# Kernel optimization log

Hardware: AMD Instinct MI355X
Metric: run time of the kernel (lower is better)

Reference implementation:

```python
import jax, jax.numpy as jnp
import numpy as np

N_NODES = 50000
N_GRAPHS = 128


def gcn_conv(x, W, b, src, dst, n_nodes):
    """PyG-style GCNConv: add self-loops, symmetric normalization, linear transform, scatter-add."""
    # linear transform first (PyG applies lin before propagate)
    h = x @ W  # [N, out]
    loop = jnp.arange(n_nodes, dtype=src.dtype)
    src_f = jnp.concatenate([src, loop])  # [E+N]
    dst_f = jnp.concatenate([dst, loop])
    # degree over destination (incl. self-loops), edge weight = 1
    deg = jax.ops.segment_sum(jnp.ones_like(src_f, dtype=h.dtype), dst_f, num_segments=n_nodes)
    dinv = jnp.where(deg > 0, jax.lax.rsqrt(deg), 0.0)
    norm = dinv[src_f] * dinv[dst_f]  # [E+N]
    msg = h[src_f] * norm[:, None]  # gather + scale
    out = jax.ops.segment_sum(msg, dst_f, num_segments=n_nodes)  # scatter-add
    return out + b


def setup_inputs() -> dict:
    key = jax.random.key(0)
    k = jax.random.split(key, 8)
    in_c, hid_c, out_c = 128, 128, 64
    x = jax.random.normal(k[0], (N_NODES, in_c), dtype=jnp.float32)
    edge_index = jax.random.randint(k[1], (2, 625000), 0, N_NODES, dtype=jnp.int64)
    batch = jnp.sort(jax.random.randint(k[2], (N_NODES,), 0, N_GRAPHS, dtype=jnp.int64))
    # Glorot-style init for GCN weights, zero bias (PyG default)
    W1 = jax.random.normal(k[3], (in_c, hid_c), dtype=jnp.float32) / np.sqrt(in_c)
    b1 = jnp.zeros((hid_c,), dtype=jnp.float32)
    W2 = jax.random.normal(k[4], (hid_c, out_c), dtype=jnp.float32) / np.sqrt(hid_c)
    b2 = jnp.zeros((out_c,), dtype=jnp.float32)
    return {"x": x, "W1": W1, "b1": b1, "W2": W2, "b2": b2,
            "edge_index": edge_index, "batch": batch}


def reference(x, W1, b1, W2, b2, edge_index, batch):
    src, dst = edge_index[0], edge_index[1]
    h = gcn_conv(x, W1, b1, src, dst, N_NODES)
    h = jax.nn.relu(h)
    h = gcn_conv(h, W2, b2, src, dst, N_NODES)  # [N, out_c]
    # global_mean_pool: segment mean over batch vector
    sums = jax.ops.segment_sum(h, batch, num_segments=N_GRAPHS)  # [G, out_c]
    counts = jax.ops.segment_sum(jnp.ones((h.shape[0],), dtype=h.dtype), batch, num_segments=N_GRAPHS)
    return sums / jnp.maximum(counts, 1.0)[:, None]
```

## Files before the change

kernel.cpp:

```cpp
#include <hip/hip_runtime.h>
#include <hip/hip_bf16.h>
#include <stdint.h>

typedef __hip_bfloat16  bf16;
typedef __hip_bfloat162 bf2;

typedef __attribute__((ext_vector_type(8))) short short8v;
typedef __attribute__((ext_vector_type(4))) float float4v;

#define KSLOT 48
#define CSTRIDE 16

static __device__ __forceinline__ uint32_t pack2(float a, float b) {
  bf2 t = __float22bfloat162_rn(make_float2(a, b));
  return *(uint32_t*)&t;
}

union U16x8 { uint32_t u[4]; uint4 q; short8v v; };

#define NB_GEMM 782
#define NB_FILL 611


__global__ void k_prep(const float* __restrict__ W1, const float* __restrict__ W2,
                       ushort* __restrict__ Ws1, ushort* __restrict__ Ws2,
                       const int* __restrict__ batch, int* __restrict__ gstart,
                       int n, int G) {
  const int tid = threadIdx.x;
  if (blockIdx.x == 0) {
    for (int idx = tid; idx < 2048; idx += 256) {
      int t = idx >> 8, c = (idx >> 6) & 3, l = idx & 63;
      int kbase = c * 32 + (l >> 4) * 8, colg = t * 16 + (l & 15);
      U16x8 u;
#pragma unroll
      for (int j = 0; j < 4; ++j)
        u.u[j] = pack2(W1[(size_t)(kbase + 2 * j) * 128 + colg],
                       W1[(size_t)(kbase + 2 * j + 1) * 128 + colg]);
      *(uint4*)&Ws1[(size_t)idx * 8] = u.q;
    }
  } else {
    for (int idx = tid; idx < 1024; idx += 256) {
      int t = idx >> 8, c = (idx >> 6) & 3, l = idx & 63;
      int kbase = c * 32 + (l >> 4) * 8, colg = t * 16 + (l & 15);
      U16x8 u;
#pragma unroll
      for (int j = 0; j < 4; ++j)
        u.u[j] = pack2(W2[(size_t)(kbase + 2 * j) * 64 + colg],
                       W2[(size_t)(kbase + 2 * j + 1) * 64 + colg]);
      *(uint4*)&Ws2[(size_t)idx * 8] = u.q;
    }
    if (tid <= G) {
      int lo = 0, hi = n;
      while (lo < hi) {
        int mid = (lo + hi) >> 1;
        if (batch[mid] < tid) lo = mid + 1; else hi = mid;
      }
      gstart[tid] = lo;
    }
  }
}


__global__ __launch_bounds__(256) void k_fused(
    const float* __restrict__ A, const ushort* __restrict__ Ws1, bf16* __restrict__ C, int n,
    const int* __restrict__ src, const int* __restrict__ dst,
    int* __restrict__ cntS, ushort* __restrict__ slots, int E) {
  __shared__ ushort Wf[2048 * 8];
  const int bid = blockIdx.x;
  const int tid = threadIdx.x;

  if (bid < NB_FILL) {
    int base = bid * 1024 + tid;
#pragma unroll
    for (int j = 0; j < 4; ++j) {
      int e = base + j * 256;
      if (e < E) {
        int d = dst[e];
        int p = atomicAdd(&cntS[d << 4], 1);
        if (p < KSLOT) slots[(size_t)d * KSLOT + p] = (ushort)src[e];
      }
    }
  } else {
    for (int idx = tid; idx < 2048; idx += 256)
      *(uint4*)&Wf[(size_t)idx * 8] = *(const uint4*)&Ws1[(size_t)idx * 8];
    __syncthreads();
    const int row0 = (bid - NB_FILL) * 64;
    const int w = tid >> 6, lane = tid & 63;
    const int m = lane & 15, q = lane >> 4;
    const int gr = row0 + w * 16 + m;
    float4v acc[8];
#pragma unroll
    for (int t = 0; t < 8; ++t) acc[t] = (float4v){0.f, 0.f, 0.f, 0.f};
    for (int c = 0; c < 4; ++c) {
      U16x8 a;
      if (gr < n) {
        const float* ap = &A[(size_t)gr * 128 + c * 32 + q * 8];
        float4 f0 = *(const float4*)ap;
        float4 f1 = *(const float4*)(ap + 4);
        a.u[0] = pack2(f0.x, f0.y); a.u[1] = pack2(f0.z, f0.w);
        a.u[2] = pack2(f1.x, f1.y); a.u[3] = pack2(f1.z, f1.w);
      } else {
        a.q = make_uint4(0, 0, 0, 0);
      }
#pragma unroll
      for (int t = 0; t < 8; ++t) {
        U16x8 b;
        b.q = *(const uint4*)&Wf[((size_t)(t * 4 + c) * 64 + lane) * 8];
        acc[t] = __builtin_amdgcn_mfma_f32_16x16x32_bf16(a.v, b.v, acc[t], 0, 0, 0);
      }
    }
#pragma unroll
    for (int reg = 0; reg < 4; ++reg) {
      int gor = row0 + w * 16 + q * 4 + reg;
      if (gor < n) {
#pragma unroll
        for (int t = 0; t < 8; ++t)
          C[(size_t)gor * 128 + t * 16 + m] = __float2bfloat16(acc[t][reg]);
      }
    }
  }
}

__global__ void k_dinv(const int* __restrict__ cntS, float* __restrict__ dinv, int n) {
  int i = blockIdx.x * blockDim.x + threadIdx.x;
  if (i < n) dinv[i] = rsqrtf((float)(cntS[i << 4] + 1));
}


__global__ __launch_bounds__(256) void k_gemm64(const bf16* __restrict__ A,
                                                const ushort* __restrict__ Ws2,
                                                bf16* __restrict__ C, int n) {
  __shared__ ushort Wf[1024 * 8];
  const int tid = threadIdx.x;
  const int row0 = blockIdx.x * 64;
  for (int idx = tid; idx < 1024; idx += 256)
    *(uint4*)&Wf[(size_t)idx * 8] = *(const uint4*)&Ws2[(size_t)idx * 8];
  __syncthreads();
  const int w = tid >> 6, lane = tid & 63;
  const int m = lane & 15, q = lane >> 4;
  const int gr = row0 + w * 16 + m;
  float4v acc[4];
#pragma unroll
  for (int t = 0; t < 4; ++t) acc[t] = (float4v){0.f, 0.f, 0.f, 0.f};
  for (int c = 0; c < 4; ++c) {
    U16x8 a;
    if (gr < n) {
      a.q = *(const uint4*)&A[(size_t)gr * 128 + c * 32 + q * 8];
    } else {
      a.q = make_uint4(0, 0, 0, 0);
    }
#pragma unroll
    for (int t = 0; t < 4; ++t) {
      U16x8 b;
      b.q = *(const uint4*)&Wf[((size_t)(t * 4 + c) * 64 + lane) * 8];
      acc[t] = __builtin_amdgcn_mfma_f32_16x16x32_bf16(a.v, b.v, acc[t], 0, 0, 0);
    }
  }
#pragma unroll
  for (int reg = 0; reg < 4; ++reg) {
    int gor = row0 + w * 16 + q * 4 + reg;
    if (gor < n) {
#pragma unroll
      for (int t = 0; t < 4; ++t)
        C[(size_t)gor * 64 + t * 16 + m] = __float2bfloat16(acc[t][reg]);
    }
  }
}


__global__ void k_agg1(const bf16* __restrict__ h, const float* __restrict__ dinv,
                       const int* __restrict__ cntS, const ushort* __restrict__ slots,
                       const float* __restrict__ b1, bf16* __restrict__ out, int n) {
  int wid = threadIdx.x >> 6, lane = threadIdx.x & 63;
  int v = blockIdx.x * 4 + wid;
  if (v >= n) return;
  const int nm1 = n - 1;
  float dv = dinv[v];
  float2 self = __bfloat1622float2(((const bf2*)(h + (size_t)v * 128))[lane]);
  float ax = self.x * dv, ay = self.y * dv;
  int deg = min(cntS[v << 4], KSLOT);
  const ushort* sl = slots + (size_t)v * KSLOT;
  for (int e = 0; e < deg; e += 8) {
    uint4 u8 = *(const uint4*)&sl[e];
    int id[8] = {(int)(u8.x & 0xffff), (int)(u8.x >> 16), (int)(u8.y & 0xffff), (int)(u8.y >> 16),
                 (int)(u8.z & 0xffff), (int)(u8.z >> 16), (int)(u8.w & 0xffff), (int)(u8.w >> 16)};
    float w[8];
#pragma unroll
    for (int j = 0; j < 8; ++j) {
      id[j] = min(id[j], nm1);
      w[j] = (e + j < deg) ? dinv[id[j]] : 0.f;
    }
    float2 g[8];
#pragma unroll
    for (int j = 0; j < 8; ++j)
      g[j] = __bfloat1622float2(((const bf2*)(h + (size_t)id[j] * 128))[lane]);
#pragma unroll
    for (int j = 0; j < 8; ++j) { ax += w[j] * g[j].x; ay += w[j] * g[j].y; }
  }
  float2 bb = ((const float2*)b1)[lane];
  float rx = fmaxf(ax * dv + bb.x, 0.f);
  float ry = fmaxf(ay * dv + bb.y, 0.f);
  ((bf2*)(out + (size_t)v * 128))[lane] = __float22bfloat162_rn(make_float2(rx, ry));
}

__global__ void k_agg2(const bf16* __restrict__ h, const float* __restrict__ dinv,
                       const int* __restrict__ cntS, const ushort* __restrict__ slots,
                       const float* __restrict__ b2, float* __restrict__ o2, int n) {
  int wid = threadIdx.x >> 6, lane = threadIdx.x & 63;
  int v = blockIdx.x * 4 + wid;
  if (v >= n) return;
  const int nm1 = n - 1;
  float dv = dinv[v];
  float acc = __bfloat162float(h[(size_t)v * 64 + lane]) * dv;
  int deg = min(cntS[v << 4], KSLOT);
  const ushort* sl = slots + (size_t)v * KSLOT;
  for (int e = 0; e < deg; e += 8) {
    uint4 u8 = *(const uint4*)&sl[e];
    int id[8] = {(int)(u8.x & 0xffff), (int)(u8.x >> 16), (int)(u8.y & 0xffff), (int)(u8.y >> 16),
                 (int)(u8.z & 0xffff), (int)(u8.z >> 16), (int)(u8.w & 0xffff), (int)(u8.w >> 16)};
    float w[8];
#pragma unroll
    for (int j = 0; j < 8; ++j) {
      id[j] = min(id[j], nm1);
      w[j] = (e + j < deg) ? dinv[id[j]] : 0.f;
    }
    float g[8];
#pragma unroll
    for (int j = 0; j < 8; ++j)
      g[j] = __bfloat162float(h[(size_t)id[j] * 64 + lane]);
#pragma unroll
    for (int j = 0; j < 8; ++j) acc += w[j] * g[j];
  }
  o2[(size_t)v * 64 + lane] = acc * dv + b2[lane];
}

__global__ void k_pool(const float* __restrict__ o2, const int* __restrict__ gstart,
                       float* __restrict__ out) {
  int g = blockIdx.x;
  int s = gstart[g], epos = gstart[g + 1];
  int lane = threadIdx.x & 63, wid = threadIdx.x >> 6;
  float acc = 0.f;
  for (int i = s + wid; i < epos; i += 4)
    acc += o2[(size_t)i * 64 + lane];
  __shared__ float red[4][64];
  red[wid][lane] = acc;
  __syncthreads();
  if (wid == 0) {
    float v = red[0][lane] + red[1][lane] + red[2][lane] + red[3][lane];
    float c = (float)max(epos - s, 1);
    out[g * 64 + lane] = v / c;
  }
}


extern "C" void kernel_launch(void* const* d_in, const int* in_sizes, int n_in,
                              void* d_out, int out_size, void* d_ws, size_t ws_size,
                              hipStream_t stream) {
  const float* x   = (const float*)d_in[0];
  const float* W1  = (const float*)d_in[1];
  const float* b1  = (const float*)d_in[2];
  const float* W2  = (const float*)d_in[3];
  const float* b2  = (const float*)d_in[4];
  const int* ei    = (const int*)d_in[5];
  const int* batch = (const int*)d_in[6];

  const int n = in_sizes[0] / 128;
  const int E = in_sizes[5] / 2;
  const int G = 128;

  const int* src = ei;
  const int* dst = ei + E;

  char* ws = (char*)d_ws;
  size_t off = 0;
  auto alloc = [&](size_t bytes) -> void* {
    void* p = ws + off;
    off = (off + bytes + 255) & ~(size_t)255;
    return p;
  };
  bf16*   h1    = (bf16*)alloc((size_t)n * 128 * 2);
  bf16*   a1    = (bf16*)alloc((size_t)n * 128 * 2);
  ushort* slots = (ushort*)alloc((size_t)n * KSLOT * 2);
  int*    cntS  = (int*)alloc((size_t)n * CSTRIDE * 4);
  float*  dinv  = (float*)alloc((size_t)n * 4);
  int*    gstart= (int*)alloc((size_t)(G + 1) * 4);
  ushort* Ws1   = (ushort*)alloc(2048 * 16);
  ushort* Ws2   = (ushort*)alloc(1024 * 16);
  bf16*   h2 = h1;
  float*  o2 = (float*)a1;
  float*  out = (float*)d_out;

  hipMemsetAsync(cntS, 0, (size_t)n * CSTRIDE * 4, stream);

  k_prep<<<2, 256, 0, stream>>>(W1, W2, Ws1, Ws2, batch, gstart, n, G);
  k_fused<<<NB_GEMM + NB_FILL, 256, 0, stream>>>(x, Ws1, h1, n, src, dst, cntS, slots, E);
  k_dinv<<<(n + 255) / 256, 256, 0, stream>>>(cntS, dinv, n);
  k_agg1<<<(n + 3) / 4, 256, 0, stream>>>(h1, dinv, cntS, slots, b1, a1, n);
  k_gemm64<<<(n + 63) / 64, 256, 0, stream>>>(a1, Ws2, h2, n);
  k_agg2<<<(n + 3) / 4, 256, 0, stream>>>(h2, dinv, cntS, slots, b2, o2, n);
  k_pool<<<G, 256, 0, stream>>>(o2, gstart, out);
}
```

Measured before the change: 211.2 us.

## Fold mean pooling into second aggregation via dense graph-by-node coefficient matrix

Pooling and the second GCN aggregation are both linear, so they are folded into one dense coefficient matrix C2[G, n]. Each entry holds the normalized edge weight times the inverse graph size, built with atomics over edges and self-loops. A blocked dot product of C2 with the second-layer features, followed by a partial-sum reduction, then replaces the per-node neighbour gather (k_agg2) and the pooling kernel. The cost is a large memset and strided reads of a 128×n float matrix, plus per-edge scattered atomics. The edge-fill loop is also retuned to 8 edges per thread over half as many blocks.

```diff
diff --git a/kernel.cpp b/kernel.cpp
--- a/kernel.cpp
+++ b/kernel.cpp
@@ -10,6 +10,7 @@
 
 #define KSLOT 48
 #define CSTRIDE 16
+#define NGR 128
 
 static __device__ __forceinline__ uint32_t pack2(float a, float b) {
   bf2 t = __float22bfloat162_rn(make_float2(a, b));
@@ -18,14 +19,15 @@
 
 union U16x8 { uint32_t u[4]; uint4 q; short8v v; };
 
+#define NB_FILL 306
 #define NB_GEMM 782
-#define NB_FILL 611
+#define NB_CF   611
 
 
 __global__ void k_prep(const float* __restrict__ W1, const float* __restrict__ W2,
                        ushort* __restrict__ Ws1, ushort* __restrict__ Ws2,
                        const int* __restrict__ batch, int* __restrict__ gstart,
-                       int n, int G) {
+                       float* __restrict__ inv_ng, int n, int G) {
   const int tid = threadIdx.x;
   if (blockIdx.x == 0) {
     for (int idx = tid; idx < 2048; idx += 256) {
@@ -39,6 +41,7 @@
       *(uint4*)&Ws1[(size_t)idx * 8] = u.q;
     }
   } else {
+    __shared__ int gs[NGR + 1];
     for (int idx = tid; idx < 1024; idx += 256) {
       int t = idx >> 8, c = (idx >> 6) & 3, l = idx & 63;
       int kbase = c * 32 + (l >> 4) * 8, colg = t * 16 + (l & 15);
@@ -56,7 +59,10 @@
         if (batch[mid] < tid) lo = mid + 1; else hi = mid;
       }
       gstart[tid] = lo;
-    }
+      gs[tid] = lo;
+    }
+    __syncthreads();
+    if (tid < G) inv_ng[tid] = 1.f / (float)max(gs[tid + 1] - gs[tid], 1);
   }
 }
 
@@ -70,9 +76,9 @@
   const int tid = threadIdx.x;
 
   if (bid < NB_FILL) {
-    int base = bid * 1024 + tid;
-#pragma unroll
-    for (int j = 0; j < 4; ++j) {
+    int base = bid * 2048 + tid;
+#pragma unroll
+    for (int j = 0; j < 8; ++j) {
       int e = base + j * 256;
       if (e < E) {
         int d = dst[e];
@@ -121,9 +127,71 @@
   }
 }
 
-__global__ void k_dinv(const int* __restrict__ cntS, float* __restrict__ dinv, int n) {
+__global__ void k_dinv(const int* __restrict__ cntS, float* __restrict__ dinv,
+                       const int* __restrict__ batch, const float* __restrict__ inv_ng,
+                       float* __restrict__ C2, int n) {
   int i = blockIdx.x * blockDim.x + threadIdx.x;
-  if (i < n) dinv[i] = rsqrtf((float)(cntS[i << 4] + 1));
+  if (i < n) {
+    float d = rsqrtf((float)(cntS[i << 4] + 1));
+    dinv[i] = d;
+    int g = batch[i];
+    atomicAdd(&C2[(size_t)g * n + i], d * d * inv_ng[g]);
+  }
+}
+
+
+__global__ __launch_bounds__(256) void k_agg1cf(
+    const bf16* __restrict__ h, const float* __restrict__ dinv,
+    const int* __restrict__ cntS, const ushort* __restrict__ slots,
+    const float* __restrict__ b1, bf16* __restrict__ out, int n,
+    const int* __restrict__ src, const int* __restrict__ dst,
+    const int* __restrict__ batch, const float* __restrict__ inv_ng,
+    float* __restrict__ C2, int E) {
+  const int bid = blockIdx.x;
+  if (bid < NB_CF) {
+    int base = bid * 1024 + threadIdx.x;
+#pragma unroll
+    for (int j = 0; j < 4; ++j) {
+      int e = base + j * 256;
+      if (e < E) {
+        int u = src[e], v = dst[e];
+        int g = batch[v];
+        float wgt = dinv[u] * dinv[v] * inv_ng[g];
+        atomicAdd(&C2[(size_t)g * n + u], wgt);
+      }
+    }
+    return;
+  }
+  int wid = threadIdx.x >> 6, lane = threadIdx.x & 63;
+  int v = (bid - NB_CF) * 4 + wid;
+  if (v >= n) return;
+  float dv = dinv[v];
+  float2 self = __bfloat1622float2(((const bf2*)(h + (size_t)v * 128))[lane]);
+  float ax = self.x * dv, ay = self.y * dv;
+  int deg = min(cntS[v << 4], KSLOT);
+  const ushort* sl = slots + (size_t)v * KSLOT;
+  for (int e = 0; e < deg; e += 8) {
+    uint4 u8 = *(const uint4*)&sl[e];
+    int id[8] = {(int)(u8.x & 0xffff), (int)(u8.x >> 16), (int)(u8.y & 0xffff), (int)(u8.y >> 16),
+                 (int)(u8.z & 0xffff), (int)(u8.z >> 16), (int)(u8.w & 0xffff), (int)(u8.w >> 16)};
+    float w[8];
+#pragma unroll
+    for (int j = 0; j < 8; ++j) {
+      bool live = (e + j < deg);
+      id[j] = live ? id[j] : v;
+      w[j] = live ? dinv[id[j]] : 0.f;
+    }
+    float2 g[8];
+#pragma unroll
+    for (int j = 0; j < 8; ++j)
+      g[j] = __bfloat1622float2(((const bf2*)(h + (size_t)id[j] * 128))[lane]);
+#pragma unroll
+    for (int j = 0; j < 8; ++j) { ax += w[j] * g[j].x; ay += w[j] * g[j].y; }
+  }
+  float2 bb = ((const float2*)b1)[lane];
+  float rx = fmaxf(ax * dv + bb.x, 0.f);
+  float ry = fmaxf(ay * dv + bb.y, 0.f);
+  ((bf2*)(out + (size_t)v * 128))[lane] = __float22bfloat162_rn(make_float2(rx, ry));
 }
 
 
@@ -168,88 +236,35 @@
 }
 
 
-__global__ void k_agg1(const bf16* __restrict__ h, const float* __restrict__ dinv,
-                       const int* __restrict__ cntS, const ushort* __restrict__ slots,
-                       const float* __restrict__ b1, bf16* __restrict__ out, int n) {
-  int wid = threadIdx.x >> 6, lane = threadIdx.x & 63;
-  int v = blockIdx.x * 4 + wid;
-  if (v >= n) return;
-  const int nm1 = n - 1;
-  float dv = dinv[v];
-  float2 self = __bfloat1622float2(((const bf2*)(h + (size_t)v * 128))[lane]);
-  float ax = self.x * dv, ay = self.y * dv;
-  int deg = min(cntS[v << 4], KSLOT);
-  const ushort* sl = slots + (size_t)v * KSLOT;
-  for (int e = 0; e < deg; e += 8) {
-    uint4 u8 = *(const uint4*)&sl[e];
-    int id[8] = {(int)(u8.x & 0xffff), (int)(u8.x >> 16), (int)(u8.y & 0xffff), (int)(u8.y >> 16),
-                 (int)(u8.z & 0xffff), (int)(u8.z >> 16), (int)(u8.w & 0xffff), (int)(u8.w >> 16)};
-    float w[8];
-#pragma unroll
-    for (int j = 0; j < 8; ++j) {
-      id[j] = min(id[j], nm1);
-      w[j] = (e + j < deg) ? dinv[id[j]] : 0.f;
-    }
-    float2 g[8];
-#pragma unroll
-    for (int j = 0; j < 8; ++j)
-      g[j] = __bfloat1622float2(((const bf2*)(h + (size_t)id[j] * 128))[lane]);
-#pragma unroll
-    for (int j = 0; j < 8; ++j) { ax += w[j] * g[j].x; ay += w[j] * g[j].y; }
-  }
-  float2 bb = ((const float2*)b1)[lane];
-  float rx = fmaxf(ax * dv + bb.x, 0.f);
-  float ry = fmaxf(ay * dv + bb.y, 0.f);
-  ((bf2*)(out + (size_t)v * 128))[lane] = __float22bfloat162_rn(make_float2(rx, ry));
-}
-
-__global__ void k_agg2(const bf16* __restrict__ h, const float* __restrict__ dinv,
-                       const int* __restrict__ cntS, const ushort* __restrict__ slots,
-                       const float* __restrict__ b2, float* __restrict__ o2, int n) {
-  int wid = threadIdx.x >> 6, lane = threadIdx.x & 63;
-  int v = blockIdx.x * 4 + wid;
-  if (v >= n) return;
-  const int nm1 = n - 1;
-  float dv = dinv[v];
-  float acc = __bfloat162float(h[(size_t)v * 64 + lane]) * dv;
-  int deg = min(cntS[v << 4], KSLOT);
-  const ushort* sl = slots + (size_t)v * KSLOT;
-  for (int e = 0; e < deg; e += 8) {
-    uint4 u8 = *(const uint4*)&sl[e];
-    int id[8] = {(int)(u8.x & 0xffff), (int)(u8.x >> 16), (int)(u8.y & 0xffff), (int)(u8.y >> 16),
-                 (int)(u8.z & 0xffff), (int)(u8.z >> 16), (int)(u8.w & 0xffff), (int)(u8.w >> 16)};
-    float w[8];
-#pragma unroll
-    for (int j = 0; j < 8; ++j) {
-      id[j] = min(id[j], nm1);
-      w[j] = (e + j < deg) ? dinv[id[j]] : 0.f;
-    }
-    float g[8];
-#pragma unroll
-    for (int j = 0; j < 8; ++j)
-      g[j] = __bfloat162float(h[(size_t)id[j] * 64 + lane]);
-#pragma unroll
-    for (int j = 0; j < 8; ++j) acc += w[j] * g[j];
-  }
-  o2[(size_t)v * 64 + lane] = acc * dv + b2[lane];
-}
-
-__global__ void k_pool(const float* __restrict__ o2, const int* __restrict__ gstart,
-                       float* __restrict__ out) {
-  int g = blockIdx.x;
-  int s = gstart[g], epos = gstart[g + 1];
-  int lane = threadIdx.x & 63, wid = threadIdx.x >> 6;
-  float acc = 0.f;
-  for (int i = s + wid; i < epos; i += 4)
-    acc += o2[(size_t)i * 64 + lane];
-  __shared__ float red[4][64];
-  red[wid][lane] = acc;
-  __syncthreads();
-  if (wid == 0) {
-    float v = red[0][lane] + red[1][lane] + red[2][lane] + red[3][lane];
-    float c = (float)max(epos - s, 1);
-    out[g * 64 + lane] = v / c;
-  }
+#define NCHUNK 196
+__global__ __launch_bounds__(256) void k_bigdot(const float* __restrict__ C2,
+                                                const bf16* __restrict__ H2,
+                                                float* __restrict__ part, int n) {
+  int b = blockIdx.x;
+  int u0 = b * NCHUNK;
+  int u1 = min(n, u0 + NCHUNK);
+  int w = threadIdx.x >> 6, lane = threadIdx.x & 63;
+  float acc[32];
+#pragma unroll
+  for (int i = 0; i < 32; ++i) acc[i] = 0.f;
+  for (int u = u0; u < u1; ++u) {
+    float hv = __bfloat162float(H2[(size_t)u * 64 + lane]);
+    const float* crow = C2 + u;
+#pragma unroll 8
+    for (int gg = 0; gg < 32; ++gg)
+      acc[gg] += crow[(size_t)(w * 32 + gg) * n] * hv;
+  }
+  float* p = part + ((size_t)b * 128 + w * 32) * 64 + lane;
+#pragma unroll
+  for (int gg = 0; gg < 32; ++gg) p[(size_t)gg * 64] = acc[gg];
+}
+
+__global__ void k_reduce(const float* __restrict__ part, const float* __restrict__ b2,
+                         float* __restrict__ out, int nblk) {
+  int idx = blockIdx.x * 256 + threadIdx.x;
+  float s = 0.f;
+  for (int b = 0; b < nblk; ++b) s += part[(size_t)b * 8192 + idx];
+  out[idx] = s + b2[idx & 63];
 }
 
 
@@ -266,7 +281,7 @@
 
   const int n = in_sizes[0] / 128;
   const int E = in_sizes[5] / 2;
-  const int G = 128;
+  const int G = NGR;
 
   const int* src = ei;
   const int* dst = ei + E;
@@ -284,19 +299,23 @@
   int*    cntS  = (int*)alloc((size_t)n * CSTRIDE * 4);
   float*  dinv  = (float*)alloc((size_t)n * 4);
   int*    gstart= (int*)alloc((size_t)(G + 1) * 4);
+  float*  invng = (float*)alloc((size_t)G * 4);
   ushort* Ws1   = (ushort*)alloc(2048 * 16);
   ushort* Ws2   = (ushort*)alloc(1024 * 16);
-  bf16*   h2 = h1;
-  float*  o2 = (float*)a1;
+  float*  C2    = (float*)alloc((size_t)G * n * 4);
+  float*  part  = (float*)alloc((size_t)256 * G * 64 * 4);
+  bf16*   H2 = h1;
   float*  out = (float*)d_out;
 
   hipMemsetAsync(cntS, 0, (size_t)n * CSTRIDE * 4, stream);
-
-  k_prep<<<2, 256, 0, stream>>>(W1, W2, Ws1, Ws2, batch, gstart, n, G);
-  k_fused<<<NB_GEMM + NB_FILL, 256, 0, stream>>>(x, Ws1, h1, n, src, dst, cntS, slots, E);
-  k_dinv<<<(n + 255) / 256, 256, 0, stream>>>(cntS, dinv, n);
-  k_agg1<<<(n + 3) / 4, 256, 0, stream>>>(h1, dinv, cntS, slots, b1, a1, n);
-  k_gemm64<<<(n + 63) / 64, 256, 0, stream>>>(a1, Ws2, h2, n);
-  k_agg2<<<(n + 3) / 4, 256, 0, stream>>>(h2, dinv, cntS, slots, b2, o2, n);
-  k_pool<<<G, 256, 0, stream>>>(o2, gstart, out);
-}
+  hipMemsetAsync(C2, 0, (size_t)G * n * 4, stream);
+
+  k_prep<<<2, 256, 0, stream>>>(W1, W2, Ws1, Ws2, batch, gstart, invng, n, G);
+  k_fused<<<NB_FILL + NB_GEMM, 256, 0, stream>>>(x, Ws1, h1, n, src, dst, cntS, slots, E);
+  k_dinv<<<(n + 255) / 256, 256, 0, stream>>>(cntS, dinv, batch, invng, C2, n);
+  k_agg1cf<<<NB_CF + (n + 3) / 4, 256, 0, stream>>>(h1, dinv, cntS, slots, b1, a1, n,
+                                                    src, dst, batch, invng, C2, E);
+  k_gemm64<<<(n + 63) / 64, 256, 0, stream>>>(a1, Ws2, H2, n);
+  k_bigdot<<<256, 256, 0, stream>>>(C2, H2, part, n);
+  k_reduce<<<32, 256, 0, stream>>>(part, b2, out, 256);
+}
```

New measurement: 711.0 us. 3.37x slower.
